# Kernel tuning notes

Measured on AMD Instinct MI355X. Metric: run time of the kernel, lower is better.

Reference implementation:

```python
import jax, jax.numpy as jnp
import numpy as np

N_NODES = 50000


def _gcn_layer(h_in, src, dst, norm, W, b, n_nodes):
    # PyG GCNConv: linear transform, then normalized scatter-add aggregation.
    h = h_in @ W                                   # [N, out]
    msg = h[src] * norm[:, None]                   # gather + scale, [E+N, out]
    out = jax.ops.segment_sum(msg, dst, num_segments=n_nodes)  # scatter-add
    return out + b


def _self_loop_norm(edge_index, n_nodes):
    # Add self loops, compute symmetric normalization deg^-1/2 (row) * deg^-1/2 (col).
    loop = jnp.arange(n_nodes, dtype=edge_index.dtype)
    src = jnp.concatenate([edge_index[0], loop])
    dst = jnp.concatenate([edge_index[1], loop])
    deg = jax.ops.segment_sum(jnp.ones_like(dst, dtype=jnp.float32), dst,
                              num_segments=n_nodes)
    dinv = jnp.where(deg > 0, jax.lax.rsqrt(deg), 0.0)
    norm = dinv[src] * dinv[dst]                   # [E+N]
    return src, dst, norm


def setup_inputs() -> dict:
    key = jax.random.key(0)
    ks = jax.random.split(key, 8)
    in_c, hid, out_c = 128, 64, 16
    x = jax.random.normal(ks[0], (N_NODES, in_c), dtype=jnp.float32)
    edge_index = jax.random.randint(ks[1], (2, 800000), 0, N_NODES, dtype=jnp.int64)
    def lin(k, fan_in, fan_out):
        lim = 1.0 / np.sqrt(fan_in)
        return jax.random.uniform(k, (fan_in, fan_out), jnp.float32, -lim, lim)
    return {
        "x": x,
        "edge_index": edge_index,
        "W1": lin(ks[2], in_c, hid), "b1": jnp.zeros((hid,), jnp.float32),
        "W2": lin(ks[3], hid, hid), "b2": jnp.zeros((hid,), jnp.float32),
        "Wm1": lin(ks[4], 2 * hid, hid), "bm1": jnp.zeros((hid,), jnp.float32),
        "Wm2": lin(ks[5], hid, out_c), "bm2": jnp.zeros((out_c,), jnp.float32),
    }


def reference(x, edge_index, W1, b1, W2, b2, Wm1, bm1, Wm2, bm2):
    n_nodes = x.shape[0]
    src, dst, norm = _self_loop_norm(edge_index, n_nodes)
    h = jax.nn.relu(_gcn_layer(x, src, dst, norm, W1, b1, n_nodes))
    h = jax.nn.relu(_gcn_layer(h, src, dst, norm, W2, b2, n_nodes))
    row, col = edge_index[0], edge_index[1]
    ef = jnp.concatenate([h[row], h[col]], axis=1)   # [E, 2*hid]
    z = jax.nn.relu(ef @ Wm1 + bm1)
    return z @ Wm2 + bm2
```

## Files before the change

kernel.cpp:

```cpp
#include <hip/hip_runtime.h>
#include <hip/hip_bf16.h>


#define IN_C 128
#define HID 64
#define OUT_C 16

__device__ __forceinline__ float rlanef(float v, int l) {
    return __uint_as_float(__builtin_amdgcn_readlane(__float_as_uint(v), l));
}


__global__ void k_init_cnt(int* __restrict__ cnt, int n) {
    int i = blockIdx.x * blockDim.x + threadIdx.x;
    if (i < n) cnt[i] = 0;
}

__global__ void k_count(const int* __restrict__ ei, int* __restrict__ cnt, int e) {
    int i = blockIdx.x * blockDim.x + threadIdx.x;
    if (i < e) atomicAdd(&cnt[ei[e + i]], 1);
}

__global__ __launch_bounds__(1024) void k_scan1(const int* __restrict__ cnt,
                                                int* __restrict__ tmp,
                                                int* __restrict__ bsum, int n) {
    __shared__ int s[1024];
    int i = blockIdx.x * 1024 + threadIdx.x;
    int v = (i < n) ? cnt[i] : 0;
    s[threadIdx.x] = v;
    __syncthreads();
    for (int off = 1; off < 1024; off <<= 1) {
        int add = (threadIdx.x >= off) ? s[threadIdx.x - off] : 0;
        __syncthreads();
        s[threadIdx.x] += add;
        __syncthreads();
    }
    if (i < n) tmp[i] = s[threadIdx.x];
    if (threadIdx.x == 1023) bsum[blockIdx.x] = s[1023];
}

__global__ void k_scan2(int* __restrict__ bsum, int nb) {
    if (blockIdx.x == 0 && threadIdx.x == 0) {
        int run = 0;
        for (int b = 0; b < nb; ++b) { int v = bsum[b]; bsum[b] = run; run += v; }
    }
}

__global__ void k_scan3(const int* __restrict__ cnt, const int* __restrict__ tmp,
                        const int* __restrict__ bsum, int* __restrict__ rowptr,
                        int* __restrict__ cur, float* __restrict__ dinv, int n, int e) {
    int i = blockIdx.x * blockDim.x + threadIdx.x;
    if (i < n) {
        int excl = tmp[i] - cnt[i] + bsum[i >> 10];
        rowptr[i] = excl;
        cur[i] = excl;
        dinv[i] = 1.0f / sqrtf((float)(cnt[i] + 1));
        if (i == 0) rowptr[n] = e;
    }
}

__global__ void k_scatter(const int* __restrict__ ei, int* __restrict__ cur,
                          int* __restrict__ csrc, int* __restrict__ cdst,
                          int* __restrict__ eorig, int e) {
    int i = blockIdx.x * blockDim.x + threadIdx.x;
    if (i < e) {
        int s = ei[i];
        int d = ei[e + i];
        int p = atomicAdd(&cur[d], 1);
        csrc[p] = s;
        cdst[p] = d;
        eorig[p] = i;
    }
}


template <int K>
__global__ __launch_bounds__(256) void k_gemm_node(const float* __restrict__ A,
                                                   const float* __restrict__ W,
                                                   const float* __restrict__ dinv,
                                                   float* __restrict__ T,
                                                   int n, int npw) {
    int lane = threadIdx.x & 63;
    int w = threadIdx.x >> 6;
    float wr[K];
#pragma unroll
    for (int k = 0; k < K; ++k) wr[k] = W[k * 64 + lane];
    int gw = blockIdx.x * 4 + w;
    int n0 = gw * npw;
    int n1 = n0 + npw; if (n1 > n) n1 = n;
#pragma unroll 1
    for (int i = n0; i < n1; ++i) {
        float a0 = A[(size_t)i * K + lane];
        float a1 = 0.f;
        if (K == 128) a1 = A[(size_t)i * K + 64 + lane];
        float acc = 0.f;
#pragma unroll
        for (int k = 0; k < 64; ++k) acc = fmaf(rlanef(a0, k), wr[k], acc);
        if (K == 128) {
#pragma unroll
            for (int k = 0; k < 64; ++k) acc = fmaf(rlanef(a1, k), wr[64 + k], acc);
        }
        T[(size_t)i * 64 + lane] = acc * dinv[i];
    }
}

__global__ __launch_bounds__(256) void k_gemm_uv(const float* __restrict__ Hm,
                                                 const float* __restrict__ Wm1,
                                                 const float* __restrict__ bm1,
                                                 float* __restrict__ ut,
                                                 float* __restrict__ vt,
                                                 int n, int npw) {
    int lane = threadIdx.x & 63;
    int w = threadIdx.x >> 6;
    float wu[64], wv[64];
#pragma unroll
    for (int k = 0; k < 64; ++k) wu[k] = Wm1[k * 64 + lane];
#pragma unroll
    for (int k = 0; k < 64; ++k) wv[k] = Wm1[(64 + k) * 64 + lane];
    float bv = bm1[lane];
    int gw = blockIdx.x * 4 + w;
    int n0 = gw * npw;
    int n1 = n0 + npw; if (n1 > n) n1 = n;
#pragma unroll 1
    for (int i = n0; i < n1; ++i) {
        float a0 = Hm[(size_t)i * 64 + lane];
        float au = 0.f, av = 0.f;
#pragma unroll
        for (int k = 0; k < 64; ++k) {
            float hb = rlanef(a0, k);
            au = fmaf(hb, wu[k], au);
            av = fmaf(hb, wv[k], av);
        }
        ut[(size_t)i * 64 + lane] = au;
        vt[(size_t)i * 64 + lane] = av + bv;
    }
}

__global__ __launch_bounds__(256) void k_agg(const float* __restrict__ T,
                                             const int* __restrict__ rowptr,
                                             const int* __restrict__ csrc,
                                             const float* __restrict__ dinv,
                                             const float* __restrict__ bias,
                                             float* __restrict__ H, int n) {
    int lane = threadIdx.x & 63;
    int w = threadIdx.x >> 6;
    int nid = blockIdx.x * 4 + w;
    if (nid >= n) return;
    float dn = dinv[nid];
    float acc = T[(size_t)nid * 64 + lane];
    int r0 = rowptr[nid], r1 = rowptr[nid + 1];
#pragma unroll 1
    for (int p0 = r0; p0 < r1; p0 += 64) {
        int m = r1 - p0; if (m > 64) m = 64;
        int sv = (lane < m) ? csrc[p0 + lane] : 0;
        if (m == 64) {
#pragma unroll
            for (int i = 0; i < 64; ++i) {
                int s = __builtin_amdgcn_readlane(sv, i);
                acc += T[(size_t)s * 64 + lane];
            }
        } else {
#pragma unroll 1
            for (int i = 0; i < m; ++i) {
                int s = __builtin_amdgcn_readlane(sv, i);
                acc += T[(size_t)s * 64 + lane];
            }
        }
    }
    H[(size_t)nid * 64 + lane] = fmaxf(fmaf(dn, acc, bias[lane]), 0.f);
}


#define RELUADD4(zq, uq, vq) \
    zq.x = fmaxf(uq.x + vq.x, 0.f); zq.y = fmaxf(uq.y + vq.y, 0.f); \
    zq.z = fmaxf(uq.z + vq.z, 0.f); zq.w = fmaxf(uq.w + vq.w, 0.f);

#define S2Q(zs, j) { \
    const float* w2 = Wm2 + (size_t)(j) * 16; \
    o0.x = fmaf(zs, w2[0],  o0.x);  o0.y = fmaf(zs, w2[1],  o0.y); \
    o0.z = fmaf(zs, w2[2],  o0.z);  o0.w = fmaf(zs, w2[3],  o0.w); \
    o1.x = fmaf(zs, w2[4],  o1.x);  o1.y = fmaf(zs, w2[5],  o1.y); \
    o1.z = fmaf(zs, w2[6],  o1.z);  o1.w = fmaf(zs, w2[7],  o1.w); \
    o2.x = fmaf(zs, w2[8],  o2.x);  o2.y = fmaf(zs, w2[9],  o2.y); \
    o2.z = fmaf(zs, w2[10], o2.z);  o2.w = fmaf(zs, w2[11], o2.w); \
    o3.x = fmaf(zs, w2[12], o3.x);  o3.y = fmaf(zs, w2[13], o3.y); \
    o3.z = fmaf(zs, w2[14], o3.z);  o3.w = fmaf(zs, w2[15], o3.w); }

__global__ __launch_bounds__(256, 4) void k_mlp(const float* __restrict__ ut,
                                                const float* __restrict__ vt,
                                                const int* __restrict__ csrc,
                                                const int* __restrict__ cdst,
                                                const int* __restrict__ eorig,
                                                const float* __restrict__ Wm2,
                                                const float* __restrict__ bm2,
                                                float* __restrict__ out,
                                                int e) {
    int p = blockIdx.x * 256 + threadIdx.x;
    bool ok = p < e;
    int idx = ok ? p : 0;
    int r = csrc[idx];
    int c = cdst[idx];
    int eo = eorig[idx];

    const float4* uq = (const float4*)(ut + (size_t)r * 64);
    const float4* vq = (const float4*)(vt + (size_t)c * 64);

    float4 u0 = uq[0],  u1 = uq[1],  u2 = uq[2],  u3 = uq[3];
    float4 u4 = uq[4],  u5 = uq[5],  u6 = uq[6],  u7 = uq[7];
    float4 u8 = uq[8],  u9 = uq[9],  u10 = uq[10], u11 = uq[11];
    float4 u12 = uq[12], u13 = uq[13], u14 = uq[14], u15 = uq[15];
    float4 v0 = vq[0],  v1 = vq[1],  v2 = vq[2],  v3 = vq[3];
    float4 v4 = vq[4],  v5 = vq[5],  v6 = vq[6],  v7 = vq[7];
    float4 v8 = vq[8],  v9 = vq[9],  v10 = vq[10], v11 = vq[11];
    float4 v12 = vq[12], v13 = vq[13], v14 = vq[14], v15 = vq[15];

    float4 z0, z1, z2, z3, z4, z5, z6, z7, z8, z9, z10, z11, z12, z13, z14, z15;
    RELUADD4(z0, u0, v0)   RELUADD4(z1, u1, v1)   RELUADD4(z2, u2, v2)   RELUADD4(z3, u3, v3)
    RELUADD4(z4, u4, v4)   RELUADD4(z5, u5, v5)   RELUADD4(z6, u6, v6)   RELUADD4(z7, u7, v7)
    RELUADD4(z8, u8, v8)   RELUADD4(z9, u9, v9)   RELUADD4(z10, u10, v10) RELUADD4(z11, u11, v11)
    RELUADD4(z12, u12, v12) RELUADD4(z13, u13, v13) RELUADD4(z14, u14, v14) RELUADD4(z15, u15, v15)

    const float4* b2q = (const float4*)bm2;
    float4 o0 = b2q[0], o1 = b2q[1], o2 = b2q[2], o3 = b2q[3];

    S2Q(z0.x, 0)   S2Q(z0.y, 1)   S2Q(z0.z, 2)   S2Q(z0.w, 3)
    S2Q(z1.x, 4)   S2Q(z1.y, 5)   S2Q(z1.z, 6)   S2Q(z1.w, 7)
    S2Q(z2.x, 8)   S2Q(z2.y, 9)   S2Q(z2.z, 10)  S2Q(z2.w, 11)
    S2Q(z3.x, 12)  S2Q(z3.y, 13)  S2Q(z3.z, 14)  S2Q(z3.w, 15)
    S2Q(z4.x, 16)  S2Q(z4.y, 17)  S2Q(z4.z, 18)  S2Q(z4.w, 19)
    S2Q(z5.x, 20)  S2Q(z5.y, 21)  S2Q(z5.z, 22)  S2Q(z5.w, 23)
    S2Q(z6.x, 24)  S2Q(z6.y, 25)  S2Q(z6.z, 26)  S2Q(z6.w, 27)
    S2Q(z7.x, 28)  S2Q(z7.y, 29)  S2Q(z7.z, 30)  S2Q(z7.w, 31)
    S2Q(z8.x, 32)  S2Q(z8.y, 33)  S2Q(z8.z, 34)  S2Q(z8.w, 35)
    S2Q(z9.x, 36)  S2Q(z9.y, 37)  S2Q(z9.z, 38)  S2Q(z9.w, 39)
    S2Q(z10.x, 40) S2Q(z10.y, 41) S2Q(z10.z, 42) S2Q(z10.w, 43)
    S2Q(z11.x, 44) S2Q(z11.y, 45) S2Q(z11.z, 46) S2Q(z11.w, 47)
    S2Q(z12.x, 48) S2Q(z12.y, 49) S2Q(z12.z, 50) S2Q(z12.w, 51)
    S2Q(z13.x, 52) S2Q(z13.y, 53) S2Q(z13.z, 54) S2Q(z13.w, 55)
    S2Q(z14.x, 56) S2Q(z14.y, 57) S2Q(z14.z, 58) S2Q(z14.w, 59)
    S2Q(z15.x, 60) S2Q(z15.y, 61) S2Q(z15.z, 62) S2Q(z15.w, 63)

    if (ok) {
        float4* op = (float4*)(out + (size_t)eo * 16);
        op[0] = o0; op[1] = o1; op[2] = o2; op[3] = o3;
    }
}


extern "C" void kernel_launch(void* const* d_in, const int* in_sizes, int n_in,
                              void* d_out, int out_size, void* d_ws, size_t ws_size,
                              hipStream_t stream) {
    const float* x   = (const float*)d_in[0];
    const int*   ei  = (const int*)d_in[1];
    const float* W1  = (const float*)d_in[2];
    const float* b1  = (const float*)d_in[3];
    const float* W2  = (const float*)d_in[4];
    const float* b2  = (const float*)d_in[5];
    const float* Wm1 = (const float*)d_in[6];
    const float* bm1 = (const float*)d_in[7];
    const float* Wm2 = (const float*)d_in[8];
    const float* bm2 = (const float*)d_in[9];
    float* out = (float*)d_out;

    int n = in_sizes[0] / IN_C;
    int e = in_sizes[1] / 2;

    char* w = (char*)d_ws;
    int* cnt    = (int*)w;                 w += (size_t)n * 4;
    int* tmp    = (int*)w;                 w += (size_t)n * 4;
    int* bsum   = (int*)w;                 w += 256 * 4;
    int* rowptr = (int*)w;                 w += (size_t)(n + 4) * 4;
    int* cur    = (int*)w;                 w += (size_t)n * 4;
    float* dinv = (float*)w;               w += (size_t)n * 4;
    int* csrc   = (int*)w;                 w += (size_t)e * 4;
    int* cdst   = (int*)w;                 w += (size_t)e * 4;
    int* eorig  = (int*)w;                 w += (size_t)e * 4;
    float* t    = (float*)w;               w += (size_t)n * HID * 4;
    float* h1   = (float*)w;               w += (size_t)n * HID * 4;
    float* h2   = (float*)w;               w += (size_t)n * HID * 4;
    float* ut   = t;
    float* vt   = h1;

    int nb_n256 = (n + 255) / 256;
    int nb_e256 = (e + 255) / 256;
    int nb_scan = (n + 1023) / 1024;

    k_init_cnt<<<nb_n256, 256, 0, stream>>>(cnt, n);
    k_count<<<nb_e256, 256, 0, stream>>>(ei, cnt, e);
    k_scan1<<<nb_scan, 1024, 0, stream>>>(cnt, tmp, bsum, n);
    k_scan2<<<1, 64, 0, stream>>>(bsum, nb_scan);
    k_scan3<<<nb_n256, 256, 0, stream>>>(cnt, tmp, bsum, rowptr, cur, dinv, n, e);
    k_scatter<<<nb_e256, 256, 0, stream>>>(ei, cur, csrc, cdst, eorig, e);

    const int NPW = 8;
    int nwaves = (n + NPW - 1) / NPW;
    int nb_gemm = (nwaves + 3) / 4;
    int nb_agg = (n + 3) / 4;
    k_gemm_node<IN_C><<<nb_gemm, 256, 0, stream>>>(x, W1, dinv, t, n, NPW);
    k_agg<<<nb_agg, 256, 0, stream>>>(t, rowptr, csrc, dinv, b1, h1, n);
    k_gemm_node<HID><<<nb_gemm, 256, 0, stream>>>(h1, W2, dinv, t, n, NPW);
    k_agg<<<nb_agg, 256, 0, stream>>>(t, rowptr, csrc, dinv, b2, h2, n);
    k_gemm_uv<<<nb_gemm, 256, 0, stream>>>(h2, Wm1, bm1, ut, vt, n, NPW);
    int nb_mlp = (e + 255) / 256;
    k_mlp<<<nb_mlp, 256, 0, stream>>>(ut, vt, csrc, cdst, eorig, Wm2, bm2, out, e);
}
```

Measured before the change: 357.7 us.

## Fuse layer-2 GEMM into aggregation, vectorize gather, pack edge arrays, warp scan

The layer-1 aggregation kernel now also applies the W2 transform, so the separate layer-2 node GEMM launch and its h1 round trip are removed. Aggregation is restructured so each wave splits edges across four 16-lane groups that gather float4 rows and reduce with xor shuffles, processing several nodes per wave. Destination and original edge index are packed into one int2 array, the MLP uses nontemporal loads and stores, and the block-sum scan becomes a wave shuffle scan. This adds register pressure (64 weight registers held per lane in the fused kernel) and limits the shuffle scan to 64 blocks.

```diff
diff --git a/kernel.cpp b/kernel.cpp
--- a/kernel.cpp
+++ b/kernel.cpp
@@ -6,8 +6,15 @@
 #define HID 64
 #define OUT_C 16
 
+typedef float f32x4 __attribute__((ext_vector_type(4)));
+
 __device__ __forceinline__ float rlanef(float v, int l) {
     return __uint_as_float(__builtin_amdgcn_readlane(__float_as_uint(v), l));
+}
+
+__device__ __forceinline__ void nt_store4(float* p, float4 v) {
+    f32x4 x = {v.x, v.y, v.z, v.w};
+    __builtin_nontemporal_store(x, (f32x4*)p);
 }
 
 
@@ -39,11 +46,15 @@
     if (threadIdx.x == 1023) bsum[blockIdx.x] = s[1023];
 }
 
-__global__ void k_scan2(int* __restrict__ bsum, int nb) {
-    if (blockIdx.x == 0 && threadIdx.x == 0) {
-        int run = 0;
-        for (int b = 0; b < nb; ++b) { int v = bsum[b]; bsum[b] = run; run += v; }
-    }
+__global__ __launch_bounds__(64) void k_scan2(int* __restrict__ bsum, int nb) {
+    int lane = threadIdx.x;
+    int v = (lane < nb) ? bsum[lane] : 0;
+    int orig = v;
+    for (int off = 1; off < 64; off <<= 1) {
+        int t = __shfl_up(v, off, 64);
+        if (lane >= off) v += t;
+    }
+    if (lane < nb) bsum[lane] = v - orig;
 }
 
 __global__ void k_scan3(const int* __restrict__ cnt, const int* __restrict__ tmp,
@@ -60,16 +71,14 @@
 }
 
 __global__ void k_scatter(const int* __restrict__ ei, int* __restrict__ cur,
-                          int* __restrict__ csrc, int* __restrict__ cdst,
-                          int* __restrict__ eorig, int e) {
+                          int* __restrict__ csrc, int2* __restrict__ cde, int e) {
     int i = blockIdx.x * blockDim.x + threadIdx.x;
     if (i < e) {
         int s = ei[i];
         int d = ei[e + i];
         int p = atomicAdd(&cur[d], 1);
         csrc[p] = s;
-        cdst[p] = d;
-        eorig[p] = i;
+        cde[p] = make_int2(d, i);
     }
 }
 
@@ -136,38 +145,89 @@
     }
 }
 
-__global__ __launch_bounds__(256) void k_agg(const float* __restrict__ T,
+
+__device__ __forceinline__ float4 agg_gather(const float* __restrict__ T,
                                              const int* __restrict__ rowptr,
                                              const int* __restrict__ csrc,
-                                             const float* __restrict__ dinv,
-                                             const float* __restrict__ bias,
-                                             float* __restrict__ H, int n) {
+                                             float dn, float4 b4,
+                                             int nid, int g, int c4) {
+    float4 acc = make_float4(0.f, 0.f, 0.f, 0.f);
+    if (g == 0) {
+        acc = *(const float4*)(T + (size_t)nid * 64 + 4 * c4);
+    }
+    int r0 = rowptr[nid], r1 = rowptr[nid + 1];
+#pragma unroll 1
+    for (int p = r0 + g; p < r1; p += 4) {
+        int s = csrc[p];
+        float4 t = *(const float4*)(T + (size_t)s * 64 + 4 * c4);
+        acc.x += t.x; acc.y += t.y; acc.z += t.z; acc.w += t.w;
+    }
+    acc.x += __shfl_xor(acc.x, 16, 64); acc.y += __shfl_xor(acc.y, 16, 64);
+    acc.z += __shfl_xor(acc.z, 16, 64); acc.w += __shfl_xor(acc.w, 16, 64);
+    acc.x += __shfl_xor(acc.x, 32, 64); acc.y += __shfl_xor(acc.y, 32, 64);
+    acc.z += __shfl_xor(acc.z, 32, 64); acc.w += __shfl_xor(acc.w, 32, 64);
+    float4 h;
+    h.x = fmaxf(fmaf(dn, acc.x, b4.x), 0.f);
+    h.y = fmaxf(fmaf(dn, acc.y, b4.y), 0.f);
+    h.z = fmaxf(fmaf(dn, acc.z, b4.z), 0.f);
+    h.w = fmaxf(fmaf(dn, acc.w, b4.w), 0.f);
+    return h;
+}
+
+__global__ __launch_bounds__(256) void k_agg_l1(const float* __restrict__ T,
+                                                const int* __restrict__ rowptr,
+                                                const int* __restrict__ csrc,
+                                                const float* __restrict__ dinv,
+                                                const float* __restrict__ bias,
+                                                const float* __restrict__ W2,
+                                                float* __restrict__ T2,
+                                                int n, int npw) {
     int lane = threadIdx.x & 63;
     int w = threadIdx.x >> 6;
-    int nid = blockIdx.x * 4 + w;
-    if (nid >= n) return;
-    float dn = dinv[nid];
-    float acc = T[(size_t)nid * 64 + lane];
-    int r0 = rowptr[nid], r1 = rowptr[nid + 1];
-#pragma unroll 1
-    for (int p0 = r0; p0 < r1; p0 += 64) {
-        int m = r1 - p0; if (m > 64) m = 64;
-        int sv = (lane < m) ? csrc[p0 + lane] : 0;
-        if (m == 64) {
-#pragma unroll
-            for (int i = 0; i < 64; ++i) {
-                int s = __builtin_amdgcn_readlane(sv, i);
-                acc += T[(size_t)s * 64 + lane];
-            }
-        } else {
-#pragma unroll 1
-            for (int i = 0; i < m; ++i) {
-                int s = __builtin_amdgcn_readlane(sv, i);
-                acc += T[(size_t)s * 64 + lane];
-            }
+    int g = lane >> 4, c4 = lane & 15;
+    float wr[64];
+#pragma unroll
+    for (int k = 0; k < 64; ++k) wr[k] = W2[k * 64 + lane];
+    float4 b4 = ((const float4*)bias)[c4];
+    int gw = blockIdx.x * 4 + w;
+    int n0 = gw * npw;
+    int n1 = n0 + npw; if (n1 > n) n1 = n;
+#pragma unroll 1
+    for (int nid = n0; nid < n1; ++nid) {
+        float dn = dinv[nid];
+        float4 h = agg_gather(T, rowptr, csrc, dn, b4, nid, g, c4);
+        float acc2 = 0.f;
+#pragma unroll
+        for (int q = 0; q < 16; ++q) {
+            acc2 = fmaf(rlanef(h.x, q), wr[4 * q + 0], acc2);
+            acc2 = fmaf(rlanef(h.y, q), wr[4 * q + 1], acc2);
+            acc2 = fmaf(rlanef(h.z, q), wr[4 * q + 2], acc2);
+            acc2 = fmaf(rlanef(h.w, q), wr[4 * q + 3], acc2);
         }
-    }
-    H[(size_t)nid * 64 + lane] = fmaxf(fmaf(dn, acc, bias[lane]), 0.f);
+        T2[(size_t)nid * 64 + lane] = acc2 * dn;
+    }
+}
+
+__global__ __launch_bounds__(256) void k_agg_l2(const float* __restrict__ T,
+                                                const int* __restrict__ rowptr,
+                                                const int* __restrict__ csrc,
+                                                const float* __restrict__ dinv,
+                                                const float* __restrict__ bias,
+                                                float* __restrict__ H,
+                                                int n, int npw) {
+    int lane = threadIdx.x & 63;
+    int w = threadIdx.x >> 6;
+    int g = lane >> 4, c4 = lane & 15;
+    float4 b4 = ((const float4*)bias)[c4];
+    int gw = blockIdx.x * 4 + w;
+    int n0 = gw * npw;
+    int n1 = n0 + npw; if (n1 > n) n1 = n;
+#pragma unroll 1
+    for (int nid = n0; nid < n1; ++nid) {
+        float dn = dinv[nid];
+        float4 h = agg_gather(T, rowptr, csrc, dn, b4, nid, g, c4);
+        if (g == 0) *(float4*)(H + (size_t)nid * 64 + 4 * c4) = h;
+    }
 }
 
 
@@ -189,8 +249,7 @@
 __global__ __launch_bounds__(256, 4) void k_mlp(const float* __restrict__ ut,
                                                 const float* __restrict__ vt,
                                                 const int* __restrict__ csrc,
-                                                const int* __restrict__ cdst,
-                                                const int* __restrict__ eorig,
+                                                const int2* __restrict__ cde,
                                                 const float* __restrict__ Wm2,
                                                 const float* __restrict__ bm2,
                                                 float* __restrict__ out,
@@ -198,9 +257,10 @@
     int p = blockIdx.x * 256 + threadIdx.x;
     bool ok = p < e;
     int idx = ok ? p : 0;
-    int r = csrc[idx];
-    int c = cdst[idx];
-    int eo = eorig[idx];
+    int r = __builtin_nontemporal_load(&csrc[idx]);
+    long long cv = __builtin_nontemporal_load((const long long*)(cde + idx));
+    int c  = (int)(cv & 0xffffffffll);
+    int eo = (int)(cv >> 32);
 
     const float4* uq = (const float4*)(ut + (size_t)r * 64);
     const float4* vq = (const float4*)(vt + (size_t)c * 64);
@@ -215,9 +275,9 @@
     float4 v12 = vq[12], v13 = vq[13], v14 = vq[14], v15 = vq[15];
 
     float4 z0, z1, z2, z3, z4, z5, z6, z7, z8, z9, z10, z11, z12, z13, z14, z15;
-    RELUADD4(z0, u0, v0)   RELUADD4(z1, u1, v1)   RELUADD4(z2, u2, v2)   RELUADD4(z3, u3, v3)
-    RELUADD4(z4, u4, v4)   RELUADD4(z5, u5, v5)   RELUADD4(z6, u6, v6)   RELUADD4(z7, u7, v7)
-    RELUADD4(z8, u8, v8)   RELUADD4(z9, u9, v9)   RELUADD4(z10, u10, v10) RELUADD4(z11, u11, v11)
+    RELUADD4(z0, u0, v0)    RELUADD4(z1, u1, v1)    RELUADD4(z2, u2, v2)    RELUADD4(z3, u3, v3)
+    RELUADD4(z4, u4, v4)    RELUADD4(z5, u5, v5)    RELUADD4(z6, u6, v6)    RELUADD4(z7, u7, v7)
+    RELUADD4(z8, u8, v8)    RELUADD4(z9, u9, v9)    RELUADD4(z10, u10, v10) RELUADD4(z11, u11, v11)
     RELUADD4(z12, u12, v12) RELUADD4(z13, u13, v13) RELUADD4(z14, u14, v14) RELUADD4(z15, u15, v15)
 
     const float4* b2q = (const float4*)bm2;
@@ -241,8 +301,11 @@
     S2Q(z15.x, 60) S2Q(z15.y, 61) S2Q(z15.z, 62) S2Q(z15.w, 63)
 
     if (ok) {
-        float4* op = (float4*)(out + (size_t)eo * 16);
-        op[0] = o0; op[1] = o1; op[2] = o2; op[3] = o3;
+        float* op = out + (size_t)eo * 16;
+        nt_store4(op + 0,  o0);
+        nt_store4(op + 4,  o1);
+        nt_store4(op + 8,  o2);
+        nt_store4(op + 12, o3);
     }
 }
 
@@ -273,13 +336,12 @@
     int* cur    = (int*)w;                 w += (size_t)n * 4;
     float* dinv = (float*)w;               w += (size_t)n * 4;
     int* csrc   = (int*)w;                 w += (size_t)e * 4;
-    int* cdst   = (int*)w;                 w += (size_t)e * 4;
-    int* eorig  = (int*)w;                 w += (size_t)e * 4;
-    float* t    = (float*)w;               w += (size_t)n * HID * 4;
-    float* h1   = (float*)w;               w += (size_t)n * HID * 4;
+    int2* cde   = (int2*)w;                w += (size_t)e * 8;
+    float* t1   = (float*)w;               w += (size_t)n * HID * 4;
+    float* t2   = (float*)w;               w += (size_t)n * HID * 4;
     float* h2   = (float*)w;               w += (size_t)n * HID * 4;
-    float* ut   = t;
-    float* vt   = h1;
+    float* ut   = t1;
+    float* vt   = t2;
 
     int nb_n256 = (n + 255) / 256;
     int nb_e256 = (e + 255) / 256;
@@ -290,17 +352,18 @@
     k_scan1<<<nb_scan, 1024, 0, stream>>>(cnt, tmp, bsum, n);
     k_scan2<<<1, 64, 0, stream>>>(bsum, nb_scan);
     k_scan3<<<nb_n256, 256, 0, stream>>>(cnt, tmp, bsum, rowptr, cur, dinv, n, e);
-    k_scatter<<<nb_e256, 256, 0, stream>>>(ei, cur, csrc, cdst, eorig, e);
+    k_scatter<<<nb_e256, 256, 0, stream>>>(ei, cur, csrc, cde, e);
 
     const int NPW = 8;
     int nwaves = (n + NPW - 1) / NPW;
     int nb_gemm = (nwaves + 3) / 4;
-    int nb_agg = (n + 3) / 4;
-    k_gemm_node<IN_C><<<nb_gemm, 256, 0, stream>>>(x, W1, dinv, t, n, NPW);
-    k_agg<<<nb_agg, 256, 0, stream>>>(t, rowptr, csrc, dinv, b1, h1, n);
-    k_gemm_node<HID><<<nb_gemm, 256, 0, stream>>>(h1, W2, dinv, t, n, NPW);
-    k_agg<<<nb_agg, 256, 0, stream>>>(t, rowptr, csrc, dinv, b2, h2, n);
+    const int NPB = 8;
+    int nb_agg = (n + 4 * NPB - 1) / (4 * NPB);
+
+    k_gemm_node<IN_C><<<nb_gemm, 256, 0, stream>>>(x, W1, dinv, t1, n, NPW);
+    k_agg_l1<<<nb_agg, 256, 0, stream>>>(t1, rowptr, csrc, dinv, b1, W2, t2, n, NPB);
+    k_agg_l2<<<nb_agg, 256, 0, stream>>>(t2, rowptr, csrc, dinv, b2, h2, n, NPB);
     k_gemm_uv<<<nb_gemm, 256, 0, stream>>>(h2, Wm1, bm1, ut, vt, n, NPW);
     int nb_mlp = (e + 255) / 256;
-    k_mlp<<<nb_mlp, 256, 0, stream>>>(ut, vt, csrc, cdst, eorig, Wm2, bm2, out, e);
-}
+    k_mlp<<<nb_mlp, 256, 0, stream>>>(ut, vt, csrc, cde, Wm2, bm2, out, e);
+}
```

Measured after the change: 406.0 us. 1.14x slower.
